# Kernel optimization log

Hardware: AMD Instinct MI355X
Metric: run time of the kernel (lower is better)

## Reference

```python
import jax, jax.numpy as jnp
import numpy as np

NUM_GROUPS = 32
EPS = 1e-5  # torch GroupNorm default


def group_norm(x, gamma, beta):
    # x: [b, c, h, w]
    b, c, h, w = x.shape
    xg = x.reshape(b, NUM_GROUPS, c // NUM_GROUPS, h, w)
    mean = xg.mean(axis=(2, 3, 4), keepdims=True)
    var = xg.var(axis=(2, 3, 4), keepdims=True)
    xg = (xg - mean) * jax.lax.rsqrt(var + EPS)
    x = xg.reshape(b, c, h, w)
    return x * gamma[None, :, None, None] + beta[None, :, None, None]


def conv1x1(x, w, bias):
    # 1x1 conv == channel matmul. x: [b,c,h,w], w: [cout,cin]
    y = jnp.einsum('bchw,dc->bdhw', x, w)
    return y + bias[None, :, None, None]


def setup_inputs() -> dict:
    key = jax.random.key(0)
    ks = jax.random.split(key, 11)
    C = 512
    scale = 1.0 / np.sqrt(C)
    x = jax.random.normal(ks[0], (4, C, 64, 64), dtype=jnp.float32)
    return {
        'x': x,
        'gamma': jnp.ones((C,), jnp.float32),
        'beta': jnp.zeros((C,), jnp.float32),
        'wq': jax.random.uniform(ks[1], (C, C), jnp.float32, -scale, scale),
        'bq': jax.random.uniform(ks[2], (C,), jnp.float32, -scale, scale),
        'wk': jax.random.uniform(ks[3], (C, C), jnp.float32, -scale, scale),
        'bk': jax.random.uniform(ks[4], (C,), jnp.float32, -scale, scale),
        'wv': jax.random.uniform(ks[5], (C, C), jnp.float32, -scale, scale),
        'bv': jax.random.uniform(ks[6], (C,), jnp.float32, -scale, scale),
        'wo': jax.random.uniform(ks[7], (C, C), jnp.float32, -scale, scale),
        'bo': jax.random.uniform(ks[8], (C,), jnp.float32, -scale, scale),
    }


def reference(x, gamma, beta, wq, bq, wk, bk, wv, bv, wo, bo):
    b, c, h, w = x.shape
    h_ = group_norm(x, gamma, beta)
    q = conv1x1(h_, wq, bq).reshape(b, c, h * w)
    k = conv1x1(h_, wk, bk).reshape(b, c, h * w)
    v = conv1x1(h_, wv, bv).reshape(b, c, h * w)
    # scores: [b, hw, hw] -- q^T k scaled by c^-0.5
    scores = jnp.einsum('bcn,bcm->bnm', q, k) * (c ** -0.5)
    attn = jax.nn.softmax(scores, axis=2)
    # h_ = v @ attn^T : [b, c, hw]
    out = jnp.einsum('bcm,bnm->bcn', v, attn).reshape(b, c, h, w)
    return x + conv1x1(out, wo, bo)
```

## Files before the change

kernel.cpp:

```cpp
#include <hip/hip_runtime.h>

typedef __bf16 bf16x8 __attribute__((ext_vector_type(8)));
typedef __bf16 bf16x4 __attribute__((ext_vector_type(4)));
typedef float floatx4 __attribute__((ext_vector_type(4)));

#define AS1(p) ((const __attribute__((address_space(1))) unsigned int*)(p))
#define AS3(p) ((__attribute__((address_space(3))) unsigned int*)(p))

__device__ __forceinline__ void async_cp16(const void* g, void* l) {
  __builtin_amdgcn_global_load_lds(AS1(g), AS3(l), 16, 0, 0);
}

template <bool OUT_F32>
__global__ __launch_bounds__(256, 2) void gemm_bt(
    const __bf16* __restrict__ A, const __bf16* __restrict__ B,
    void* __restrict__ Cv, const float* __restrict__ bias,
    const float* __restrict__ residual, const float* __restrict__ colscale,
    int lda, int ldb, int ldc, long sA, long sB, long sC, long sR, int K,
    int bias_mode, float scale, int swz) {
  __shared__ alignas(16) __bf16 As[128 * 32];
  __shared__ alignas(16) __bf16 Bs[128 * 32];

  const int t = threadIdx.x;
  const int bz = blockIdx.z;
  int bx = blockIdx.x, by = blockIdx.y;
  if (swz) {
    const int xcd = bx & 7, idx = bx >> 3;
    by = xcd + (idx >> 2) * 8;
    bx = idx & 3;
  }
  const int m0 = by * 128;
  const int n0 = bx * 128;

  const __bf16* Ab = A + (size_t)bz * sA;
  const __bf16* Bb = B + (size_t)bz * sB;

  const int sr = t >> 2;
  const int sc = t & 3;
  const __bf16* gA0 = Ab + (size_t)(m0 + sr) * lda + sc * 8;
  const __bf16* gA1 = gA0 + (size_t)64 * lda;
  const __bf16* gB0 = Bb + (size_t)(n0 + sr) * ldb + sc * 8;
  const __bf16* gB1 = gB0 + (size_t)64 * ldb;
  __bf16* lA0 = &As[t * 8];
  __bf16* lA1 = &As[(t + 256) * 8];
  __bf16* lB0 = &Bs[t * 8];
  __bf16* lB1 = &Bs[(t + 256) * 8];

  const int lane = t & 63;
  const int wv = t >> 6;
  const int wm = (wv & 1) * 64;
  const int wn = (wv >> 1) * 64;
  const int l15 = lane & 15;
  const int kg = lane >> 4;

  int aoff[4], boff[4];
#pragma unroll
  for (int i = 0; i < 4; ++i) aoff[i] = (wm + i * 16 + l15) * 32 + kg * 8;
#pragma unroll
  for (int j = 0; j < 4; ++j) boff[j] = (wn + j * 16 + l15) * 32 + kg * 8;

  floatx4 acc[4][4] = {};

  const int KT = K >> 5;
  for (int kt = 0; kt < KT; ++kt) {
    const size_t ko = (size_t)kt * 32;
    async_cp16(gA0 + ko, lA0);
    async_cp16(gA1 + ko, lA1);
    async_cp16(gB0 + ko, lB0);
    async_cp16(gB1 + ko, lB1);
    __syncthreads();
    bf16x8 af[4], bfr[4];
#pragma unroll
    for (int i = 0; i < 4; ++i) af[i] = *(const bf16x8*)&As[aoff[i]];
#pragma unroll
    for (int j = 0; j < 4; ++j) bfr[j] = *(const bf16x8*)&Bs[boff[j]];
#pragma unroll
    for (int i = 0; i < 4; ++i)
#pragma unroll
      for (int j = 0; j < 4; ++j)
        acc[i][j] = __builtin_amdgcn_mfma_f32_16x16x32_bf16(af[i], bfr[j],
                                                            acc[i][j], 0, 0, 0);
    __syncthreads();
  }

  const int r0 = m0 + wm + (kg << 2);
  const int c0 = n0 + wn + l15;
#pragma unroll
  for (int i = 0; i < 4; ++i) {
#pragma unroll
    for (int r = 0; r < 4; ++r) {
      const int row = r0 + i * 16 + r;
      float brow = 0.f;
      if (bias_mode == 1) brow = bias[row];
#pragma unroll
      for (int j = 0; j < 4; ++j) {
        const int col = c0 + j * 16;
        float v = acc[i][j][r];
        if (OUT_F32 && colscale) v *= colscale[(size_t)bz * 4096 + col];
        if (bias_mode == 1) v += brow;
        v *= scale;
        const size_t off = (size_t)row * ldc + col;
        if (OUT_F32) {
          float* Cf = (float*)Cv + (size_t)bz * sC;
          if (residual) v += residual[(size_t)bz * sR + off];
          Cf[off] = v;
        } else {
          __bf16* Cb = (__bf16*)Cv + (size_t)bz * sC;
          Cb[off] = (__bf16)v;
        }
      }
    }
  }
}

__global__ __launch_bounds__(256, 2) void gemm_small(
    const __bf16* __restrict__ A0, const __bf16* __restrict__ B0,
    __bf16* __restrict__ C0, const __bf16* __restrict__ A1,
    const __bf16* __restrict__ B1, __bf16* __restrict__ C1, float scale0) {
  __shared__ alignas(16) __bf16 As[128 * 32];
  __shared__ alignas(16) __bf16 Bs[128 * 32];

  const int t = threadIdx.x;
  const int z = blockIdx.z;
  const __bf16* A = z ? A1 : A0;
  const __bf16* B = z ? B1 : B0;
  __bf16* C = z ? C1 : C0;
  const float scale = z ? 1.0f : scale0;
  const int m0 = blockIdx.y * 128;
  const int n0 = blockIdx.x * 128;

  const int sr = t >> 2;
  const int sc = t & 3;
  const __bf16* gA0 = A + (size_t)(m0 + sr) * 512 + sc * 8;
  const __bf16* gA1 = gA0 + (size_t)64 * 512;
  const __bf16* gB0 = B + (size_t)(n0 + sr) * 512 + sc * 8;
  const __bf16* gB1 = gB0 + (size_t)64 * 512;
  __bf16* lA0 = &As[t * 8];
  __bf16* lA1 = &As[(t + 256) * 8];
  __bf16* lB0 = &Bs[t * 8];
  __bf16* lB1 = &Bs[(t + 256) * 8];

  const int lane = t & 63;
  const int wvv = t >> 6;
  const int wm = (wvv & 1) * 64;
  const int wn = (wvv >> 1) * 64;
  const int l15 = lane & 15;
  const int kg = lane >> 4;

  int aoff[4], boff[4];
#pragma unroll
  for (int i = 0; i < 4; ++i) aoff[i] = (wm + i * 16 + l15) * 32 + kg * 8;
#pragma unroll
  for (int j = 0; j < 4; ++j) boff[j] = (wn + j * 16 + l15) * 32 + kg * 8;

  floatx4 acc[4][4] = {};

  for (int kt = 0; kt < 16; ++kt) {
    const size_t ko = (size_t)kt * 32;
    async_cp16(gA0 + ko, lA0);
    async_cp16(gA1 + ko, lA1);
    async_cp16(gB0 + ko, lB0);
    async_cp16(gB1 + ko, lB1);
    __syncthreads();
    bf16x8 af[4], bfr[4];
#pragma unroll
    for (int i = 0; i < 4; ++i) af[i] = *(const bf16x8*)&As[aoff[i]];
#pragma unroll
    for (int j = 0; j < 4; ++j) bfr[j] = *(const bf16x8*)&Bs[boff[j]];
#pragma unroll
    for (int i = 0; i < 4; ++i)
#pragma unroll
      for (int j = 0; j < 4; ++j)
        acc[i][j] = __builtin_amdgcn_mfma_f32_16x16x32_bf16(af[i], bfr[j],
                                                            acc[i][j], 0, 0, 0);
    __syncthreads();
  }

  const int r0 = m0 + wm + (kg << 2);
  const int c0 = n0 + wn + l15;
#pragma unroll
  for (int i = 0; i < 4; ++i)
#pragma unroll
    for (int r = 0; r < 4; ++r) {
      const int row = r0 + i * 16 + r;
#pragma unroll
      for (int j = 0; j < 4; ++j)
        C[(size_t)row * 512 + c0 + j * 16] = (__bf16)(acc[i][j][r] * scale);
    }
}

__global__ __launch_bounds__(256, 2) void gemm_qk(
    const __bf16* __restrict__ G, const __bf16* __restrict__ Ht,
    const float* __restrict__ wvec, const float* __restrict__ sred,
    const float* __restrict__ gn2, __bf16* __restrict__ SP,
    float* __restrict__ Lpart) {
  __shared__ alignas(16) __bf16 As[128 * 32];
  __shared__ alignas(16) __bf16 Bs[128 * 32];
  __shared__ float smq[128];
  __shared__ float smf[256];

  const int t = threadIdx.x;
  const int bz = blockIdx.z;
  const int m0 = blockIdx.x * 128;
  const int n0 = blockIdx.y * 128;
  const long sH = 2097152;

  const __bf16* Ab = G + (size_t)bz * sH;
  const __bf16* Bb = Ht + (size_t)bz * sH;

  const int sr = t >> 2;
  const int sc = t & 3;
  const __bf16* gA0 = Ab + (size_t)(n0 + sr) * 512 + sc * 8;
  const __bf16* gA1 = gA0 + (size_t)64 * 512;
  const __bf16* gB0 = Bb + (size_t)(m0 + sr) * 512 + sc * 8;
  const __bf16* gB1 = gB0 + (size_t)64 * 512;
  __bf16* lA0 = &As[t * 8];
  __bf16* lA1 = &As[(t + 256) * 8];
  __bf16* lB0 = &Bs[t * 8];
  __bf16* lB1 = &Bs[(t + 256) * 8];

  const int lane = t & 63;
  const int wv = t >> 6;
  const int wm = (wv & 1) * 64;
  const int wn = (wv >> 1) * 64;
  const int l15 = lane & 15;
  const int kg = lane >> 4;

  if (t < 128) {
    const float Hs = sqrtf(sred[0]);
    const float Ws = sred[1];
    smq[t] = sqrtf(gn2[(size_t)bz * 4096 + n0 + t]) * Hs + Ws;
  }

  int aoff[4], boff[4];
#pragma unroll
  for (int i = 0; i < 4; ++i) aoff[i] = (wm + i * 16 + l15) * 32 + kg * 8;
#pragma unroll
  for (int j = 0; j < 4; ++j) boff[j] = (wn + j * 16 + l15) * 32 + kg * 8;

  floatx4 acc[4][4] = {};

  for (int kt = 0; kt < 16; ++kt) {
    const size_t ko = (size_t)kt * 32;
    async_cp16(gA0 + ko, lA0);
    async_cp16(gA1 + ko, lA1);
    async_cp16(gB0 + ko, lB0);
    async_cp16(gB1 + ko, lB1);
    __syncthreads();
    bf16x8 af[4], bfr[4];
#pragma unroll
    for (int i = 0; i < 4; ++i) af[i] = *(const bf16x8*)&As[aoff[i]];
#pragma unroll
    for (int j = 0; j < 4; ++j) bfr[j] = *(const bf16x8*)&Bs[boff[j]];
#pragma unroll
    for (int i = 0; i < 4; ++i)
#pragma unroll
      for (int j = 0; j < 4; ++j)
        acc[i][j] = __builtin_amdgcn_mfma_f32_16x16x32_bf16(af[i], bfr[j],
                                                            acc[i][j], 0, 0, 0);
    __syncthreads();
  }

  float wv4[4];
#pragma unroll
  for (int j = 0; j < 4; ++j)
    wv4[j] = wvec[(size_t)bz * 4096 + m0 + wn + j * 16 + l15];

  __bf16* Sb = SP + (size_t)bz * 16777216;
  const int wnh = wv >> 1;
#pragma unroll
  for (int i = 0; i < 4; ++i) {
#pragma unroll
    for (int r = 0; r < 4; ++r) {
      const int rl = wm + i * 16 + (kg << 2) + r;
      const float Mh = smq[rl];
      const size_t rowbase = (size_t)(n0 + rl) * 4096 + m0 + wn;
      float se = 0.f;
#pragma unroll
      for (int j = 0; j < 4; ++j) {
        const float p = __expf(acc[i][j][r] + wv4[j] - Mh);
        se += p;
        Sb[rowbase + j * 16 + l15] = (__bf16)p;
      }
#pragma unroll
      for (int off = 1; off < 16; off <<= 1) se += __shfl_xor(se, off);
      if (l15 == 0) smf[wnh * 128 + rl] = se;
    }
  }
  __syncthreads();
  if (t < 128)
    Lpart[((size_t)bz * 4096 + n0 + t) * 32 + blockIdx.x] =
        smf[t] + smf[128 + t];
}

__global__ __launch_bounds__(256) void gnorm_kernel(const __bf16* __restrict__ G,
                                                    float* __restrict__ gn2) {
  const int t = threadIdx.x;
  const int row = blockIdx.x * 4 + (t >> 6);
  const int lane = t & 63;
  const bf16x8 g = *(const bf16x8*)(G + (size_t)row * 512 + lane * 8);
  float n2 = 0.f;
#pragma unroll
  for (int k = 0; k < 8; ++k) {
    const float f = (float)g[k];
    n2 += f * f;
  }
#pragma unroll
  for (int off = 32; off; off >>= 1) n2 += __shfl_down(n2, off);
  if (lane == 0) gn2[row] = n2;
}

__global__ __launch_bounds__(256) void lsum_kernel(const float* __restrict__ Lp,
                                                   float* __restrict__ invL) {
  const int row = blockIdx.x * 256 + threadIdx.x;
  const float* p = Lp + (size_t)row * 32;
  float L = 0.f;
#pragma unroll
  for (int j = 0; j < 32; ++j) L += p[j];
  invL[row] = 1.0f / L;
}

__global__ __launch_bounds__(256) void reduce_kernel(
    const float* __restrict__ hn2, const float* __restrict__ wvec,
    float* __restrict__ sred) {
  const int t = threadIdx.x;
  const floatx4* h4 = (const floatx4*)hn2;
  const floatx4* w4 = (const floatx4*)wvec;
  float mh = 0.f, mw = -1e30f;
  for (int i = t; i < 4096; i += 256) {
    const floatx4 a = h4[i], b = w4[i];
#pragma unroll
    for (int k = 0; k < 4; ++k) {
      mh = fmaxf(mh, a[k]);
      mw = fmaxf(mw, b[k]);
    }
  }
#pragma unroll
  for (int off = 32; off; off >>= 1) {
    mh = fmaxf(mh, __shfl_down(mh, off));
    mw = fmaxf(mw, __shfl_down(mw, off));
  }
  __shared__ float red[8];
  if ((t & 63) == 0) {
    red[t >> 6] = mh;
    red[4 + (t >> 6)] = mw;
  }
  __syncthreads();
  if (t == 0) {
    sred[0] = fmaxf(fmaxf(red[0], red[1]), fmaxf(red[2], red[3]));
    sred[1] = fmaxf(fmaxf(red[4], red[5]), fmaxf(red[6], red[7]));
  }
}

__global__ __launch_bounds__(256) void gn_stats(const float* __restrict__ x,
                                                float* __restrict__ part) {
  const int t = threadIdx.x;
  const size_t base = (size_t)blockIdx.x * 8192;
  const floatx4* xp = (const floatx4*)(x + base);
  float s = 0.f, ss = 0.f;
#pragma unroll
  for (int i = 0; i < 8; ++i) {
    floatx4 v = xp[t + i * 256];
#pragma unroll
    for (int k = 0; k < 4; ++k) {
      s += v[k];
      ss += v[k] * v[k];
    }
  }
#pragma unroll
  for (int off = 32; off; off >>= 1) {
    s += __shfl_down(s, off);
    ss += __shfl_down(ss, off);
  }
  __shared__ float red[8];
  if ((t & 63) == 0) {
    red[t >> 6] = s;
    red[4 + (t >> 6)] = ss;
  }
  __syncthreads();
  if (t == 0) {
    part[blockIdx.x * 2] = red[0] + red[1] + red[2] + red[3];
    part[blockIdx.x * 2 + 1] = red[4] + red[5] + red[6] + red[7];
  }
}

__global__ __launch_bounds__(256) void gn_xform(const float* __restrict__ x,
                                                const float* __restrict__ part,
                                                const float* __restrict__ gamma,
                                                const float* __restrict__ beta,
                                                __bf16* __restrict__ Ht,
                                                __bf16* __restrict__ Hc) {
  __shared__ float tile[64][65];
  __shared__ float lsc[64], lsh[64];
  const int t = threadIdx.x;
  const int b = blockIdx.z;
  const int c0 = blockIdx.y * 64;
  const int n0 = blockIdx.x * 64;

  if (t < 64) {
    const int ch = c0 + t;
    const int bg = b * 32 + (ch >> 4);
    float s = 0.f, ss = 0.f;
#pragma unroll
    for (int k = 0; k < 8; ++k) {
      s += part[(bg * 8 + k) * 2];
      ss += part[(bg * 8 + k) * 2 + 1];
    }
    const float mean = s * (1.f / 65536.f);
    const float var = ss * (1.f / 65536.f) - mean * mean;
    const float rstd = rsqrtf(var + 1e-5f);
    const float g = gamma[ch] * rstd;
    lsc[t] = g;
    lsh[t] = beta[ch] - mean * g;
  }
  __syncthreads();

#pragma unroll
  for (int i = 0; i < 4; ++i) {
    const int slot = i * 256 + t;
    const int c = slot >> 4;
    const int nc = (slot & 15) * 4;
    const int ch = c0 + c;
    const floatx4 v =
        *(const floatx4*)&x[((size_t)b * 512 + ch) * 4096 + n0 + nc];
    const float scl = lsc[c];
    const float shf = lsh[c];
    bf16x4 hv;
#pragma unroll
    for (int k = 0; k < 4; ++k) {
      const float f = v[k] * scl + shf;
      tile[c][nc + k] = f;
      hv[k] = (__bf16)f;
    }
    *(bf16x4*)&Hc[((size_t)b * 512 + ch) * 4096 + n0 + nc] = hv;
  }
  __syncthreads();
#pragma unroll
  for (int i = 0; i < 4; ++i) {
    const int slot = i * 256 + t;
    const int n = slot >> 4;
    const int cc = (slot & 15) * 4;
    bf16x4 o;
#pragma unroll
    for (int k = 0; k < 4; ++k) o[k] = (__bf16)tile[cc + k][n];
    *(bf16x4*)&Ht[((size_t)b * 4096 + n0 + n) * 512 + c0 + cc] = o;
  }
}

__global__ __launch_bounds__(256) void cvt_kernel(const float* w0,
                                                  const float* w1,
                                                  const float* w2,
                                                  const float* w3, __bf16* o0,
                                                  __bf16* o1, __bf16* o2,
                                                  __bf16* o3) {
  __shared__ float tile[64][65];
  const int t = threadIdx.x;
  const int z = blockIdx.z;
  const int r0 = blockIdx.y * 64;
  const int d0 = blockIdx.x * 64;

  if (z == 3) {
#pragma unroll
    for (int i = 0; i < 4; ++i) {
      const int slot = i * 256 + t;
      const int r = slot >> 4;
      const int cc = (slot & 15) * 4;
      const floatx4 v = *(const floatx4*)&w3[(size_t)(r0 + r) * 512 + d0 + cc];
      bf16x4 ov;
#pragma unroll
      for (int k = 0; k < 4; ++k) ov[k] = (__bf16)v[k];
      *(bf16x4*)&o3[(size_t)(r0 + r) * 512 + d0 + cc] = ov;
    }
    return;
  }
  const float* w = z == 0 ? w0 : z == 1 ? w1 : w2;
  __bf16* o = z == 0 ? o0 : z == 1 ? o1 : o2;
#pragma unroll
  for (int i = 0; i < 4; ++i) {
    const int slot = i * 256 + t;
    const int r = slot >> 4;
    const int cc = (slot & 15) * 4;
    const floatx4 v = *(const floatx4*)&w[(size_t)(r0 + r) * 512 + d0 + cc];
#pragma unroll
    for (int k = 0; k < 4; ++k) tile[r][cc + k] = v[k];
  }
  __syncthreads();
#pragma unroll
  for (int i = 0; i < 4; ++i) {
    const int slot = i * 256 + t;
    const int d = slot >> 4;
    const int cc = (slot & 15) * 4;
    bf16x4 ov;
#pragma unroll
    for (int k = 0; k < 4; ++k) ov[k] = (__bf16)tile[cc + k][d];
    *(bf16x4*)&o[(size_t)(d0 + d) * 512 + r0 + cc] = ov;
  }
}

__global__ __launch_bounds__(256) void prep_kernel(
    const float* __restrict__ wk, const float* __restrict__ bq,
    const float* __restrict__ bk, const float* __restrict__ wo,
    const float* __restrict__ bv, const float* __restrict__ bo,
    float* __restrict__ uq, float* __restrict__ bias2, float qscale) {
  const int bidx = blockIdx.x;
  const int t = threadIdx.x;
  float s = 0.f;
  if (bidx < 512) {
    s = bq[t] * wk[(size_t)t * 512 + bidx] +
        bq[t + 256] * wk[(size_t)(t + 256) * 512 + bidx];
  } else if (bidx < 1024) {
    const int d = bidx - 512;
    s = wo[(size_t)d * 512 + t] * bv[t] +
        wo[(size_t)d * 512 + t + 256] * bv[t + 256];
  } else {
    s = bq[t] * bk[t] + bq[t + 256] * bk[t + 256];
  }
#pragma unroll
  for (int off = 32; off; off >>= 1) s += __shfl_down(s, off);
  __shared__ float red[4];
  if ((t & 63) == 0) red[t >> 6] = s;
  __syncthreads();
  if (t == 0) {
    const float tot = red[0] + red[1] + red[2] + red[3];
    if (bidx < 512)
      uq[bidx] = qscale * tot;
    else if (bidx < 1024)
      bias2[bidx - 512] = tot + bo[bidx - 512];
    else
      uq[512] = qscale * tot;
  }
}

__global__ __launch_bounds__(256) void wvec_kernel(const __bf16* __restrict__ Ht,
                                                   const float* __restrict__ uq,
                                                   float* __restrict__ wvec,
                                                   float* __restrict__ hn2) {
  const int t = threadIdx.x;
  const int row = blockIdx.x * 4 + (t >> 6);
  const int lane = t & 63;
  const bf16x8 h = *(const bf16x8*)(Ht + (size_t)row * 512 + lane * 8);
  const floatx4 u0 = *(const floatx4*)(uq + lane * 8);
  const floatx4 u1 = *(const floatx4*)(uq + lane * 8 + 4);
  float s = 0.f, n2 = 0.f;
#pragma unroll
  for (int k = 0; k < 4; ++k) {
    const float f0 = (float)h[k], f1 = (float)h[4 + k];
    s += f0 * u0[k] + f1 * u1[k];
    n2 += f0 * f0 + f1 * f1;
  }
#pragma unroll
  for (int off = 32; off; off >>= 1) {
    s += __shfl_down(s, off);
    n2 += __shfl_down(n2, off);
  }
  if (lane == 0) {
    wvec[row] = s + uq[512];
    hn2[row] = n2;
  }
}

extern "C" void kernel_launch(void* const* d_in, const int* in_sizes, int n_in,
                              void* d_out, int out_size, void* d_ws,
                              size_t ws_size, hipStream_t stream) {
  const float* x = (const float*)d_in[0];
  const float* gamma = (const float*)d_in[1];
  const float* beta = (const float*)d_in[2];
  const float* wq = (const float*)d_in[3];
  const float* bq = (const float*)d_in[4];
  const float* wk = (const float*)d_in[5];
  const float* bk = (const float*)d_in[6];
  const float* wv = (const float*)d_in[7];
  const float* bv = (const float*)d_in[8];
  const float* wo = (const float*)d_in[9];
  const float* bo = (const float*)d_in[10];

  __bf16* ws = (__bf16*)d_ws;
  __bf16* wqT = ws;
  __bf16* wkT = wqT + 262144;
  __bf16* wvT = wkT + 262144;
  __bf16* woB = wvT + 262144;
  __bf16* AqkT = woB + 262144;
  __bf16* Wb = AqkT + 262144;
  __bf16* Ht = Wb + 262144;
  __bf16* Hc = Ht + 8388608;
  __bf16* G = Hc + 8388608;
  __bf16* Z = G + 8388608;
  __bf16* SP = Z + 8388608;
  float* Lpart = (float*)(SP + 67108864);
  float* invL = Lpart + 524288;
  float* hn2 = invL + 16384;
  float* wvec = hn2 + 16384;
  float* uq = wvec + 16384;
  float* bias2 = uq + 1024;
  float* sred = bias2 + 512;
  float* gn2 = sred + 64;
  const size_t need = ((size_t)(6 * 262144 + 4 * 8388608 + 67108864)) * 2 +
                      (524288 + 4 * 16384 + 1024 + 512 + 128) * 4;
  if (ws_size < need) return;

  float* part = (float*)SP;

  const float qscale = 0.04419417382415922f;
  const long sH = 2097152;

  cvt_kernel<<<dim3(8, 8, 4), 256, 0, stream>>>(wq, wk, wv, wo, wqT, wkT, wvT,
                                                woB);
  prep_kernel<<<1025, 256, 0, stream>>>(wk, bq, bk, wo, bv, bo, uq, bias2,
                                        qscale);
  gemm_small<<<dim3(4, 4, 2), 256, 0, stream>>>(wkT, wqT, AqkT, woB, wvT, Wb,
                                                qscale);

  gn_stats<<<1024, 256, 0, stream>>>(x, part);
  gn_xform<<<dim3(64, 8, 4), 256, 0, stream>>>(x, part, gamma, beta, Ht, Hc);

  wvec_kernel<<<4096, 256, 0, stream>>>(Ht, uq, wvec, hn2);

  gemm_bt<false><<<dim3(4, 32, 4), 256, 0, stream>>>(
      Ht, AqkT, G, nullptr, nullptr, nullptr, 512, 512, 512, sH, 0, sH, 0, 512,
      0, 1.0f, 0);

  gnorm_kernel<<<4096, 256, 0, stream>>>(G, gn2);

  reduce_kernel<<<1, 256, 0, stream>>>(hn2, wvec, sred);

  gemm_qk<<<dim3(32, 32, 4), 256, 0, stream>>>(G, Ht, wvec, sred, gn2, SP,
                                               Lpart);
  lsum_kernel<<<64, 256, 0, stream>>>(Lpart, invL);

  gemm_bt<false><<<dim3(128, 1, 4), 256, 0, stream>>>(
      SP, Hc, Z, nullptr, nullptr, nullptr, 4096, 4096, 512, 16777216, sH, sH,
      0, 4096, 0, 1.0f, 1);

  gemm_bt<true><<<dim3(32, 4, 4), 256, 0, stream>>>(
      Wb, Z, d_out, bias2, x, invL, 512, 512, 4096, 0, sH, sH, sH, 512, 1,
      1.0f, 0);
}
```

Measured before the change: 396.9 us.

## Rewrite QK score GEMM with 256x256 tiles, 8 waves and triple-buffered LDS

Replaces the 128x128 single-buffered score GEMM with a 256x256-tile, 512-thread kernel that keeps three LDS stages of async global-to-LDS loads in flight and double-buffers register fragments, using explicit waitcnt, barriers and setprio around the MFMA block. Larger tiles raise data reuse per loaded byte, and the pipeline is meant to hide load latency that the old load-sync-compute loop exposed. The partial row-sum layout drops from 32 to 16 column blocks, so lsum is updated to match. In exchange it uses more LDS and registers per block, launches a quarter as many blocks, and depends on hand-counted vmcnt values being correct.

```diff
diff --git a/kernel.cpp b/kernel.cpp
--- a/kernel.cpp
+++ b/kernel.cpp
@@ -189,77 +189,103 @@
     }
 }
 
-__global__ __launch_bounds__(256, 2) void gemm_qk(
+__global__ __launch_bounds__(512) void gemm_qk8(
     const __bf16* __restrict__ G, const __bf16* __restrict__ Ht,
     const float* __restrict__ wvec, const float* __restrict__ sred,
     const float* __restrict__ gn2, __bf16* __restrict__ SP,
     float* __restrict__ Lpart) {
-  __shared__ alignas(16) __bf16 As[128 * 32];
-  __shared__ alignas(16) __bf16 Bs[128 * 32];
-  __shared__ float smq[128];
-  __shared__ float smf[256];
+  __shared__ alignas(16) __bf16 Ab[3][8192];
+  __shared__ alignas(16) __bf16 Bb[3][8192];
+  __shared__ float smq[256];
+  __shared__ float smf[1024];
 
   const int t = threadIdx.x;
   const int bz = blockIdx.z;
-  const int m0 = blockIdx.x * 128;
-  const int n0 = blockIdx.y * 128;
+  const int m0 = blockIdx.x * 256;
+  const int n0 = blockIdx.y * 256;
   const long sH = 2097152;
 
-  const __bf16* Ab = G + (size_t)bz * sH;
-  const __bf16* Bb = Ht + (size_t)bz * sH;
-
-  const int sr = t >> 2;
-  const int sc = t & 3;
-  const __bf16* gA0 = Ab + (size_t)(n0 + sr) * 512 + sc * 8;
-  const __bf16* gA1 = gA0 + (size_t)64 * 512;
-  const __bf16* gB0 = Bb + (size_t)(m0 + sr) * 512 + sc * 8;
-  const __bf16* gB1 = gB0 + (size_t)64 * 512;
-  __bf16* lA0 = &As[t * 8];
-  __bf16* lA1 = &As[(t + 256) * 8];
-  __bf16* lB0 = &Bs[t * 8];
-  __bf16* lB1 = &Bs[(t + 256) * 8];
+  const __bf16* Gb = G + (size_t)bz * sH;
+  const __bf16* Hb = Ht + (size_t)bz * sH;
+
+  const int rbase = ((t >> 5) << 3) + (t & 7);
+  const int cc8 = ((t >> 3) & 3) * 8;
+  const __bf16* gA = Gb + (size_t)(n0 + rbase) * 512 + cc8;
+  const __bf16* gB = Hb + (size_t)(m0 + rbase) * 512 + cc8;
+
+  if (t < 256) {
+    smq[t] = sqrtf(gn2[(size_t)bz * 4096 + n0 + t]) * sqrtf(sred[0]) + sred[1];
+  }
+  __builtin_amdgcn_sched_barrier(0);
 
   const int lane = t & 63;
-  const int wv = t >> 6;
-  const int wm = (wv & 1) * 64;
-  const int wn = (wv >> 1) * 64;
+  const int wid = t >> 6;
+  const int wm = (wid & 1) * 128;
+  const int wn = (wid >> 1) * 64;
   const int l15 = lane & 15;
   const int kg = lane >> 4;
 
-  if (t < 128) {
-    const float Hs = sqrtf(sred[0]);
-    const float Ws = sred[1];
-    smq[t] = sqrtf(gn2[(size_t)bz * 4096 + n0 + t]) * Hs + Ws;
-  }
-
-  int aoff[4], boff[4];
-#pragma unroll
-  for (int i = 0; i < 4; ++i) aoff[i] = (wm + i * 16 + l15) * 32 + kg * 8;
-#pragma unroll
-  for (int j = 0; j < 4; ++j) boff[j] = (wn + j * 16 + l15) * 32 + kg * 8;
-
-  floatx4 acc[4][4] = {};
-
-  for (int kt = 0; kt < 16; ++kt) {
-    const size_t ko = (size_t)kt * 32;
-    async_cp16(gA0 + ko, lA0);
-    async_cp16(gA1 + ko, lA1);
-    async_cp16(gB0 + ko, lB0);
-    async_cp16(gB1 + ko, lB1);
-    __syncthreads();
-    bf16x8 af[4], bfr[4];
-#pragma unroll
-    for (int i = 0; i < 4; ++i) af[i] = *(const bf16x8*)&As[aoff[i]];
-#pragma unroll
-    for (int j = 0; j < 4; ++j) bfr[j] = *(const bf16x8*)&Bs[boff[j]];
-#pragma unroll
-    for (int i = 0; i < 4; ++i)
-#pragma unroll
-      for (int j = 0; j < 4; ++j)
-        acc[i][j] = __builtin_amdgcn_mfma_f32_16x16x32_bf16(af[i], bfr[j],
-                                                            acc[i][j], 0, 0, 0);
-    __syncthreads();
-  }
+  const int lodd = ((l15 >> 3) << 8) + kg * 64 + (l15 & 7) * 8;
+  const int abase = wm * 32 + lodd;
+  const int bbase = wn * 32 + lodd;
+
+#define QK_STAGE(KT, S)                                       \
+  {                                                           \
+    const size_t ko = (size_t)(KT) * 32;                      \
+    async_cp16(gA + ko, &Ab[S][t * 8]);                       \
+    async_cp16(gA + ko + 65536, &Ab[S][4096 + t * 8]);        \
+    async_cp16(gB + ko, &Bb[S][t * 8]);                       \
+    async_cp16(gB + ko + 65536, &Bb[S][4096 + t * 8]);        \
+  }
+
+  floatx4 acc[8][4] = {};
+  bf16x8 fa0[8], fb0[4], fa1[8], fb1[4];
+
+  QK_STAGE(0, 0);
+  QK_STAGE(1, 1);
+  QK_STAGE(2, 2);
+  asm volatile("s_waitcnt vmcnt(4)" ::: "memory");
+  __builtin_amdgcn_sched_barrier(0);
+  __builtin_amdgcn_s_barrier();
+#pragma unroll
+  for (int i = 0; i < 8; ++i) fa0[i] = *(const bf16x8*)&Ab[0][abase + i * 512];
+#pragma unroll
+  for (int j = 0; j < 4; ++j) fb0[j] = *(const bf16x8*)&Bb[0][bbase + j * 512];
+  asm volatile("s_waitcnt lgkmcnt(0)" ::: "memory");
+  __builtin_amdgcn_sched_barrier(0);
+  __builtin_amdgcn_s_barrier();
+
+#define QK_BODY(KT, FA, FB, NA, NB)                                         \
+  {                                                                         \
+    if ((KT) + 3 < 16) QK_STAGE((KT) + 3, ((KT) % 3));                      \
+    if ((KT) + 1 < 16) {                                                    \
+      const int s_ = ((KT) + 1) % 3;                                        \
+      _Pragma("unroll") for (int i = 0; i < 8; ++i) NA[i] =                 \
+          *(const bf16x8*)&Ab[s_][abase + i * 512];                         \
+      _Pragma("unroll") for (int j = 0; j < 4; ++j) NB[j] =                 \
+          *(const bf16x8*)&Bb[s_][bbase + j * 512];                         \
+    }                                                                       \
+    __builtin_amdgcn_s_setprio(1);                                          \
+    _Pragma("unroll") for (int i = 0; i < 8; ++i)                           \
+        _Pragma("unroll") for (int j = 0; j < 4; ++j) acc[i][j] =           \
+            __builtin_amdgcn_mfma_f32_16x16x32_bf16(FA[i], FB[j],           \
+                                                    acc[i][j], 0, 0, 0);    \
+    __builtin_amdgcn_s_setprio(0);                                          \
+    if ((KT) <= 12)                                                         \
+      asm volatile("s_waitcnt vmcnt(4) lgkmcnt(0)" ::: "memory");           \
+    else                                                                    \
+      asm volatile("s_waitcnt vmcnt(0) lgkmcnt(0)" ::: "memory");           \
+    __builtin_amdgcn_sched_barrier(0);                                      \
+    __builtin_amdgcn_s_barrier();                                           \
+  }
+
+#pragma unroll
+  for (int kt = 0; kt < 16; kt += 2) {
+    QK_BODY(kt, fa0, fb0, fa1, fb1);
+    QK_BODY(kt + 1, fa1, fb1, fa0, fb0);
+  }
+#undef QK_BODY
+#undef QK_STAGE
 
   float wv4[4];
 #pragma unroll
@@ -267,9 +293,9 @@
     wv4[j] = wvec[(size_t)bz * 4096 + m0 + wn + j * 16 + l15];
 
   __bf16* Sb = SP + (size_t)bz * 16777216;
-  const int wnh = wv >> 1;
-#pragma unroll
-  for (int i = 0; i < 4; ++i) {
+  const int qn = wid >> 1;
+#pragma unroll
+  for (int i = 0; i < 8; ++i) {
 #pragma unroll
     for (int r = 0; r < 4; ++r) {
       const int rl = wm + i * 16 + (kg << 2) + r;
@@ -284,13 +310,13 @@
       }
 #pragma unroll
       for (int off = 1; off < 16; off <<= 1) se += __shfl_xor(se, off);
-      if (l15 == 0) smf[wnh * 128 + rl] = se;
+      if (l15 == 0) smf[qn * 256 + rl] = se;
     }
   }
   __syncthreads();
-  if (t < 128)
-    Lpart[((size_t)bz * 4096 + n0 + t) * 32 + blockIdx.x] =
-        smf[t] + smf[128 + t];
+  if (t < 256)
+    Lpart[((size_t)bz * 4096 + n0 + t) * 16 + blockIdx.x] =
+        smf[t] + smf[256 + t] + smf[512 + t] + smf[768 + t];
 }
 
 __global__ __launch_bounds__(256) void gnorm_kernel(const __bf16* __restrict__ G,
@@ -313,10 +339,10 @@
 __global__ __launch_bounds__(256) void lsum_kernel(const float* __restrict__ Lp,
                                                    float* __restrict__ invL) {
   const int row = blockIdx.x * 256 + threadIdx.x;
-  const float* p = Lp + (size_t)row * 32;
+  const float* p = Lp + (size_t)row * 16;
   float L = 0.f;
 #pragma unroll
-  for (int j = 0; j < 32; ++j) L += p[j];
+  for (int j = 0; j < 16; ++j) L += p[j];
   invL[row] = 1.0f / L;
 }
 
@@ -623,8 +649,8 @@
 
   reduce_kernel<<<1, 256, 0, stream>>>(hn2, wvec, sred);
 
-  gemm_qk<<<dim3(32, 32, 4), 256, 0, stream>>>(G, Ht, wvec, sred, gn2, SP,
-                                               Lpart);
+  gemm_qk8<<<dim3(16, 16, 4), 512, 0, stream>>>(G, Ht, wvec, sred, gn2, SP,
+                                                Lpart);
   lsum_kernel<<<64, 256, 0, stream>>>(Lpart, invL);
 
   gemm_bt<false><<<dim3(128, 1, 4), 256, 0, stream>>>(
```

Result: slower. 414.1 us (+4.3%).
